# Performance work log

Hardware: AMD Instinct MI355X
Metric: run time of the kernel (lower is better)

The kernel has to match this reference:

```python
import jax, jax.numpy as jnp
import numpy as np

N_EMBD = 1024
N_HEAD = 16
HEAD_SIZE = N_EMBD // N_HEAD  # 64
EPS = 1e-5


def layer_norm(x, gamma, beta):
    mu = jnp.mean(x, axis=-1, keepdims=True)
    var = jnp.var(x, axis=-1, keepdims=True)
    return (x - mu) * jax.lax.rsqrt(var + EPS) * gamma + beta


def setup_inputs() -> dict:
    key = jax.random.key(0)
    ks = jax.random.split(key, 12)
    B, T, C, H, hs = 4, 2048, N_EMBD, N_HEAD, HEAD_SIZE
    s = 0.02
    return {
        "x": jax.random.normal(ks[0], (B, T, C), jnp.float32),
        # per-head projections, stacked over heads: [H, C, hs]
        "Wq": jax.random.normal(ks[1], (H, C, hs), jnp.float32) * s,
        "Wk": jax.random.normal(ks[2], (H, C, hs), jnp.float32) * s,
        "Wv": jax.random.normal(ks[3], (H, C, hs), jnp.float32) * s,
        "Wo": jax.random.normal(ks[4], (C, C), jnp.float32) * s,
        "bo": jnp.zeros((C,), jnp.float32),
        "W1": jax.random.normal(ks[5], (C, 4 * C), jnp.float32) * s,
        "b1": jnp.zeros((4 * C,), jnp.float32),
        "W2": jax.random.normal(ks[6], (4 * C, C), jnp.float32) * s,
        "b2": jnp.zeros((C,), jnp.float32),
        "g1": jnp.ones((C,), jnp.float32),
        "be1": jnp.zeros((C,), jnp.float32),
        "g2": jnp.ones((C,), jnp.float32),
        "be2": jnp.zeros((C,), jnp.float32),
    }


def reference(x, Wq, Wk, Wv, Wo, bo, W1, b1, W2, b2, g1, be1, g2, be2):
    B, T, C = x.shape
    # --- self-attention branch (pre-LN) ---
    h = layer_norm(x, g1, be1)
    q = jnp.einsum("btc,hcd->bhtd", h, Wq)
    k = jnp.einsum("btc,hcd->bhtd", h, Wk)
    v = jnp.einsum("btc,hcd->bhtd", h, Wv)
    scale = HEAD_SIZE ** -0.5
    wei = jnp.einsum("bhtd,bhsd->bhts", q, k) * scale  # [B,H,T,T]
    causal = jnp.tril(jnp.ones((T, T), bool))
    wei = jnp.where(causal, wei, -jnp.inf)
    wei = jax.nn.softmax(wei, axis=-1)
    attn = jnp.einsum("bhts,bhsd->bhtd", wei, v)  # [B,H,T,hs]
    # concat heads -> [B,T,C]
    attn = attn.transpose(0, 2, 1, 3).reshape(B, T, C)
    x = x + attn @ Wo + bo
    # --- MLP branch (pre-LN) ---
    h = layer_norm(x, g2, be2)
    h = jax.nn.relu(h @ W1 + b1) @ W2 + b2
    return x + h
```

## Files before the change

kernel.cpp:

```cpp
#include <hip/hip_runtime.h>
#include <cstdint>
#include <cstddef>


typedef unsigned short u16;
typedef __attribute__((ext_vector_type(8))) __bf16 bf16x8;
typedef __attribute__((ext_vector_type(4))) short s16x4;
typedef __attribute__((ext_vector_type(4))) float f32x4;

#if defined(__has_builtin)
#if __has_builtin(__builtin_amdgcn_global_load_lds)
#define HAS_GLL 1
#endif
#endif

#define QSCALE 0.18033688011112042f

__device__ __forceinline__ u16 f2bf(float f) {
  union { float f; unsigned int u; } c; c.f = f;
  unsigned int u = c.u;
  u += 0x7FFFu + ((u >> 16) & 1u);
  return (u16)(u >> 16);
}
__device__ __forceinline__ u16 f2bf_fast(float f) {
  union { float f; unsigned int u; } c; c.f = f;
  return (u16)((c.u + 0x8000u) >> 16);
}

__device__ __forceinline__ float fexp2(float x) {
#if defined(__HIP_DEVICE_COMPILE__)
#if defined(__has_builtin) && __has_builtin(__builtin_amdgcn_exp2f)
  return __builtin_amdgcn_exp2f(x);
#else
  float r;
  asm("v_exp_f32 %0, %1" : "=v"(r) : "v"(x));
  return r;
#endif
#else
  return x;
#endif
}

__device__ __forceinline__ f32x4 mfma_pv(s16x4 a, s16x4 b, f32x4 c) {
#if defined(__HIP_DEVICE_COMPILE__)
#if defined(__has_builtin) && __has_builtin(__builtin_amdgcn_mfma_f32_16x16x16bf16_1k)
  return __builtin_amdgcn_mfma_f32_16x16x16bf16_1k(a, b, c, 0, 0, 0);
#else
  f32x4 d;
  asm volatile("v_mfma_f32_16x16x16_bf16 %0, %1, %2, %3"
               : "=v"(d) : "v"(a), "v"(b), "v"(c));
  return d;
#endif
#else
  (void)a; (void)b;
  return c;
#endif
}

__device__ __forceinline__ void stage16(const u16* g, u16* l, int lane) {
#ifdef HAS_GLL
  __builtin_amdgcn_global_load_lds(
      (const __attribute__((address_space(1))) uint32_t*)(g),
      (__attribute__((address_space(3))) uint32_t*)(l), 16, 0, 0);
#else
  *(int4*)(l + lane * 8) = *(const int4*)g;
#endif
}

__global__ __launch_bounds__(256) void ln_k(const float* __restrict__ x,
                                            const float* __restrict__ g,
                                            const float* __restrict__ be,
                                            u16* __restrict__ out) {
  const int row = blockIdx.x;
  const int t = threadIdx.x;
  const float4 v = ((const float4*)(x + (size_t)row * 1024))[t];
  float s = v.x + v.y + v.z + v.w;
  float s2 = v.x * v.x + v.y * v.y + v.z * v.z + v.w * v.w;
#pragma unroll
  for (int off = 32; off > 0; off >>= 1) {
    s += __shfl_down(s, off);
    s2 += __shfl_down(s2, off);
  }
  __shared__ float red[8];
  if ((t & 63) == 0) { red[t >> 6] = s; red[4 + (t >> 6)] = s2; }
  __syncthreads();
  const float ts = red[0] + red[1] + red[2] + red[3];
  const float ts2 = red[4] + red[5] + red[6] + red[7];
  const float mu = ts * (1.0f / 1024.0f);
  const float var = ts2 * (1.0f / 1024.0f) - mu * mu;
  const float rstd = rsqrtf(var + 1e-5f);
  const float4 gv = ((const float4*)g)[t];
  const float4 bv = ((const float4*)be)[t];
  u16* op = out + (size_t)row * 1024 + t * 4;
  op[0] = f2bf((v.x - mu) * rstd * gv.x + bv.x);
  op[1] = f2bf((v.y - mu) * rstd * gv.y + bv.y);
  op[2] = f2bf((v.z - mu) * rstd * gv.z + bv.z);
  op[3] = f2bf((v.w - mu) * rstd * gv.w + bv.w);
}

__global__ __launch_bounds__(256) void transpose_k(const float* __restrict__ in,
                                                   u16* __restrict__ out,
                                                   int R, int Cc) {
  __shared__ float tile[32][33];
  const size_t base = (size_t)blockIdx.z * R * Cc;
  const int r0 = blockIdx.x * 32, c0 = blockIdx.y * 32;
  const int tx = threadIdx.x & 31, ty = threadIdx.x >> 5;
  const float* ip = in + base;
  u16* op = out + base;
#pragma unroll
  for (int i = 0; i < 32; i += 8)
    tile[ty + i][tx] = ip[(size_t)(r0 + ty + i) * Cc + c0 + tx];
  __syncthreads();
#pragma unroll
  for (int i = 0; i < 32; i += 8)
    op[(size_t)(c0 + ty + i) * R + r0 + tx] = f2bf(tile[tx][ty + i]);
}

template <int MODE>
__global__ __launch_bounds__(256, 3) void gemm_k(
    const u16* __restrict__ A, const u16* __restrict__ Bt,
    const float* __restrict__ bias, const float* __restrict__ resid,
    void* __restrict__ out0, void* __restrict__ out1, void* __restrict__ out2,
    int M, int N, int K) {
  __shared__ u16 As[128 * 32];
  __shared__ u16 Bs[128 * 32];
  const int tid = threadIdx.x;
  const int lane = tid & 63;
  const int w = tid >> 6;
  const int wm = w & 1, wn = w >> 1;
  const int l15 = lane & 15, lq = lane >> 4;
  const int m0 = blockIdx.x * 128, n0 = blockIdx.y * 128;
  const int srow = lane >> 2, scol = (lane & 3) * 8;

  f32x4 acc[4][4] = {};

  const u16* gA0 = A  + (size_t)(m0 + w * 32 + srow) * K + scol;
  const u16* gA1 = gA0 + (size_t)16 * K;
  const u16* gB0 = Bt + (size_t)(n0 + w * 32 + srow) * K + scol;
  const u16* gB1 = gB0 + (size_t)16 * K;
  u16* lA0 = &As[(w * 32) * 32];
  u16* lA1 = &As[(w * 32 + 16) * 32];
  u16* lB0 = &Bs[(w * 32) * 32];
  u16* lB1 = &Bs[(w * 32 + 16) * 32];

  for (int k0 = 0; k0 < K; k0 += 32) {
    __syncthreads();
    stage16(gA0 + k0, lA0, lane);
    stage16(gA1 + k0, lA1, lane);
    stage16(gB0 + k0, lB0, lane);
    stage16(gB1 + k0, lB1, lane);
    __syncthreads();
    bf16x8 af[4], bfr[4];
#pragma unroll
    for (int i = 0; i < 4; ++i)
      af[i] = *(const bf16x8*)&As[(wm * 64 + i * 16 + l15) * 32 + lq * 8];
#pragma unroll
    for (int j = 0; j < 4; ++j)
      bfr[j] = *(const bf16x8*)&Bs[(wn * 64 + j * 16 + l15) * 32 + lq * 8];
#pragma unroll
    for (int i = 0; i < 4; ++i)
#pragma unroll
      for (int j = 0; j < 4; ++j)
        acc[i][j] = __builtin_amdgcn_mfma_f32_16x16x32_bf16(af[i], bfr[j], acc[i][j], 0, 0, 0);
  }

#pragma unroll
  for (int i = 0; i < 4; ++i) {
    const int mbase = m0 + wm * 64 + i * 16 + lq * 4;
#pragma unroll
    for (int j = 0; j < 4; ++j) {
      const int ncol = n0 + wn * 64 + j * 16 + l15;
#pragma unroll
      for (int r = 0; r < 4; ++r) {
        const float v = acc[i][j][r];
        const int m = mbase + r;
        if (MODE == 0) {
          const int which = ncol >> 10;
          const int hh = (ncol >> 6) & 15;
          const int dd = ncol & 63;
          const int tt = m & 2047;
          const size_t bhb = (size_t)((m >> 11) * 16 + hh) * 131072;
          if (which == 0) {
            ((u16*)out0)[bhb + tt * 64 + dd] = f2bf(v * QSCALE);
          } else if (which == 1) {
            ((u16*)out1)[bhb + (tt >> 4) * 1024 + (dd >> 5) * 512 +
                         ((((dd & 31) >> 3) * 16 + (tt & 15)) << 3) + (dd & 7)] = f2bf(v);
          } else {
            ((u16*)out2)[bhb + (dd >> 4) * 32768 + (tt >> 4) * 256 +
                         (((dd & 15) + (((tt >> 2) & 3)) * 16) << 2) + (tt & 3)] = f2bf(v);
          }
        } else if (MODE == 1 || MODE == 3) {
          ((float*)out0)[(size_t)m * N + ncol] =
              v + bias[ncol] + resid[(size_t)m * N + ncol];
        } else {
          const float t2 = v + bias[ncol];
          ((u16*)out0)[(size_t)m * N + ncol] = f2bf(t2 > 0.0f ? t2 : 0.0f);
        }
      }
    }
  }
}

__global__ __launch_bounds__(256) void flash_k(const u16* __restrict__ q,
                                               const u16* __restrict__ k,
                                               const u16* __restrict__ vt,
                                               u16* __restrict__ attn) {
  const int bh = blockIdx.x;
  const int qblk = 31 - blockIdx.y;
  const int bb = bh >> 4, hh = bh & 15;
  const int tid = threadIdx.x;
  const int lane = tid & 63, wid = tid >> 6;
  const int l15 = lane & 15, lq = lane >> 4;
  const int q0w = qblk * 64 + wid * 16;

  const u16* qrow = q + ((size_t)bh * 2048 + q0w + l15) * 64 + lq * 8;
  const bf16x8 qb0 = *(const bf16x8*)qrow;
  const bf16x8 qb1 = *(const bf16x8*)(qrow + 32);

  const u16* kC = k + (size_t)bh * 131072 + lane * 8;
  const u16* vC = vt + (size_t)bh * 131072 + lane * 4;

  f32x4 o[4] = {};
  float l_acc = 0.0f;

#pragma unroll 4
  for (int j0 = 0; j0 < q0w; j0 += 16) {
    const u16* kp = kC + j0 * 64;
    f32x4 st = {};
    st = __builtin_amdgcn_mfma_f32_16x16x32_bf16(*(const bf16x8*)kp, qb0, st, 0, 0, 0);
    st = __builtin_amdgcn_mfma_f32_16x16x32_bf16(*(const bf16x8*)(kp + 512), qb1, st, 0, 0, 0);

    float p0 = fexp2(st[0]), p1 = fexp2(st[1]);
    float p2 = fexp2(st[2]), p3 = fexp2(st[3]);
    l_acc += (p0 + p1) + (p2 + p3);
    s16x4 pf;
    pf[0] = (short)f2bf_fast(p0); pf[1] = (short)f2bf_fast(p1);
    pf[2] = (short)f2bf_fast(p2); pf[3] = (short)f2bf_fast(p3);

#pragma unroll
    for (int dt = 0; dt < 4; ++dt) {
      const s16x4 va = *(const s16x4*)(vC + dt * 32768 + j0 * 16);
      o[dt] = mfma_pv(va, pf, o[dt]);
    }
  }

  {
    const int j0 = q0w;
    const u16* kp = kC + j0 * 64;
    f32x4 st = {};
    st = __builtin_amdgcn_mfma_f32_16x16x32_bf16(*(const bf16x8*)kp, qb0, st, 0, 0, 0);
    st = __builtin_amdgcn_mfma_f32_16x16x32_bf16(*(const bf16x8*)(kp + 512), qb1, st, 0, 0, 0);
#pragma unroll
    for (int r = 0; r < 4; ++r)
      if (lq * 4 + r > l15) st[r] = -1e30f;

    float p0 = fexp2(st[0]), p1 = fexp2(st[1]);
    float p2 = fexp2(st[2]), p3 = fexp2(st[3]);
    l_acc += (p0 + p1) + (p2 + p3);
    s16x4 pf;
    pf[0] = (short)f2bf_fast(p0); pf[1] = (short)f2bf_fast(p1);
    pf[2] = (short)f2bf_fast(p2); pf[3] = (short)f2bf_fast(p3);

#pragma unroll
    for (int dt = 0; dt < 4; ++dt) {
      const s16x4 va = *(const s16x4*)(vC + dt * 32768 + j0 * 16);
      o[dt] = mfma_pv(va, pf, o[dt]);
    }
  }

  l_acc += __shfl_xor(l_acc, 16);
  l_acc += __shfl_xor(l_acc, 32);
  const float rl = 1.0f / l_acc;

  u16* op = attn + ((size_t)bb * 2048 + q0w + l15) * 1024 + hh * 64 + lq * 4;
#pragma unroll
  for (int dt = 0; dt < 4; ++dt) {
    union { s16x4 v; u16 a[4]; } pk;
#pragma unroll
    for (int r = 0; r < 4; ++r) pk.a[r] = f2bf(o[dt][r] * rl);
    *(s16x4*)(op + dt * 16) = pk.v;
  }
}

extern "C" void kernel_launch(void* const* d_in, const int* in_sizes, int n_in,
                              void* d_out, int out_size, void* d_ws, size_t ws_size,
                              hipStream_t stream) {
  const float* x   = (const float*)d_in[0];
  const float* Wq  = (const float*)d_in[1];
  const float* Wk  = (const float*)d_in[2];
  const float* Wv  = (const float*)d_in[3];
  const float* Wo  = (const float*)d_in[4];
  const float* bo  = (const float*)d_in[5];
  const float* W1  = (const float*)d_in[6];
  const float* b1  = (const float*)d_in[7];
  const float* W2  = (const float*)d_in[8];
  const float* b2  = (const float*)d_in[9];
  const float* g1  = (const float*)d_in[10];
  const float* be1 = (const float*)d_in[11];
  const float* g2  = (const float*)d_in[12];
  const float* be2 = (const float*)d_in[13];
  float* out = (float*)d_out;

  char* ws = (char*)d_ws;
  u16* Wqkv_t = (u16*)(ws + 0);
  u16* Wo_t   = (u16*)(ws + 6291456);
  u16* W1_t   = (u16*)(ws + 8388608);
  u16* W2_t   = (u16*)(ws + 16777216);
  u16* hbuf   = (u16*)(ws + 25165824);
  float* x2   = (float*)(ws + 41943040);
  u16* vtb    = (u16*)(ws + 41943040);
  u16* qb     = (u16*)(ws + 75497472);
  u16* kb     = (u16*)(ws + 92274688);
  u16* attnb  = (u16*)(ws + 109051904);
  u16* a1     = (u16*)(ws + 75497472);

  dim3 blk(256);

  transpose_k<<<dim3(32, 2, 16),  blk, 0, stream>>>(Wq, Wqkv_t,            1024, 64);
  transpose_k<<<dim3(32, 2, 16),  blk, 0, stream>>>(Wk, Wqkv_t + 1048576,  1024, 64);
  transpose_k<<<dim3(32, 2, 16),  blk, 0, stream>>>(Wv, Wqkv_t + 2097152,  1024, 64);
  transpose_k<<<dim3(32, 32, 1),  blk, 0, stream>>>(Wo, Wo_t,              1024, 1024);
  transpose_k<<<dim3(32, 128, 1), blk, 0, stream>>>(W1, W1_t,              1024, 4096);
  transpose_k<<<dim3(128, 32, 1), blk, 0, stream>>>(W2, W2_t,              4096, 1024);

  ln_k<<<8192, blk, 0, stream>>>(x, g1, be1, hbuf);
  gemm_k<0><<<dim3(64, 24), blk, 0, stream>>>(hbuf, Wqkv_t, nullptr, nullptr,
                                              qb, kb, vtb, 8192, 3072, 1024);
  flash_k<<<dim3(64, 32), blk, 0, stream>>>(qb, kb, vtb, attnb);
  gemm_k<1><<<dim3(64, 8), blk, 0, stream>>>(attnb, Wo_t, bo, x,
                                             x2, nullptr, nullptr, 8192, 1024, 1024);
  ln_k<<<8192, blk, 0, stream>>>(x2, g2, be2, hbuf);
  gemm_k<2><<<dim3(64, 32), blk, 0, stream>>>(hbuf, W1_t, b1, nullptr,
                                              a1, nullptr, nullptr, 8192, 4096, 1024);
  gemm_k<3><<<dim3(64, 8), blk, 0, stream>>>(a1, W2_t, b2, x2,
                                             out, nullptr, nullptr, 8192, 1024, 4096);
}
```

Baseline: 530.4 us.

## Process two query tiles per wave in flash attention to reuse K/V loads

Each wave of the flash kernel now handles 32 query rows (two 16-row tiles) instead of 16, so every K and V fragment loaded from global memory feeds two sets of MFMAs. The grid halves along the query dimension and a second diagonal tile is handled separately for the upper query tile. MFMA sections are wrapped in s_setprio hints and launch bounds request 4 blocks per CU. This doubles accumulator register use and produces fewer, larger blocks, which may worsen load balance across the causal triangle.

New measurement: 492.2 us. -7.2%, faster.

```diff
diff --git a/kernel.cpp b/kernel.cpp
--- a/kernel.cpp
+++ b/kernel.cpp
@@ -201,84 +201,162 @@
   }
 }
 
-__global__ __launch_bounds__(256) void flash_k(const u16* __restrict__ q,
-                                               const u16* __restrict__ k,
-                                               const u16* __restrict__ vt,
-                                               u16* __restrict__ attn) {
+__global__ __launch_bounds__(256, 4) void flash_k(const u16* __restrict__ q,
+                                                  const u16* __restrict__ k,
+                                                  const u16* __restrict__ vt,
+                                                  u16* __restrict__ attn) {
   const int bh = blockIdx.x;
-  const int qblk = 31 - blockIdx.y;
+  const int qblk = 15 - blockIdx.y;
   const int bb = bh >> 4, hh = bh & 15;
   const int tid = threadIdx.x;
   const int lane = tid & 63, wid = tid >> 6;
   const int l15 = lane & 15, lq = lane >> 4;
-  const int q0w = qblk * 64 + wid * 16;
-
-  const u16* qrow = q + ((size_t)bh * 2048 + q0w + l15) * 64 + lq * 8;
-  const bf16x8 qb0 = *(const bf16x8*)qrow;
-  const bf16x8 qb1 = *(const bf16x8*)(qrow + 32);
+  const int q0w = qblk * 128 + wid * 32;
+
+  const u16* qrowA = q + ((size_t)bh * 2048 + q0w + l15) * 64 + lq * 8;
+  const bf16x8 qA0 = *(const bf16x8*)qrowA;
+  const bf16x8 qA1 = *(const bf16x8*)(qrowA + 32);
+  const u16* qrowB = qrowA + 16 * 64;
+  const bf16x8 qB0 = *(const bf16x8*)qrowB;
+  const bf16x8 qB1 = *(const bf16x8*)(qrowB + 32);
 
   const u16* kC = k + (size_t)bh * 131072 + lane * 8;
   const u16* vC = vt + (size_t)bh * 131072 + lane * 4;
 
-  f32x4 o[4] = {};
-  float l_acc = 0.0f;
-
-#pragma unroll 4
-  for (int j0 = 0; j0 < q0w; j0 += 16) {
-    const u16* kp = kC + j0 * 64;
-    f32x4 st = {};
-    st = __builtin_amdgcn_mfma_f32_16x16x32_bf16(*(const bf16x8*)kp, qb0, st, 0, 0, 0);
-    st = __builtin_amdgcn_mfma_f32_16x16x32_bf16(*(const bf16x8*)(kp + 512), qb1, st, 0, 0, 0);
-
-    float p0 = fexp2(st[0]), p1 = fexp2(st[1]);
-    float p2 = fexp2(st[2]), p3 = fexp2(st[3]);
-    l_acc += (p0 + p1) + (p2 + p3);
-    s16x4 pf;
-    pf[0] = (short)f2bf_fast(p0); pf[1] = (short)f2bf_fast(p1);
-    pf[2] = (short)f2bf_fast(p2); pf[3] = (short)f2bf_fast(p3);
-
-#pragma unroll
-    for (int dt = 0; dt < 4; ++dt) {
-      const s16x4 va = *(const s16x4*)(vC + dt * 32768 + j0 * 16);
-      o[dt] = mfma_pv(va, pf, o[dt]);
-    }
+  f32x4 oA[4] = {}, oB[4] = {};
+  float lA = 0.0f, lB = 0.0f;
+
+  const int nt = q0w >> 4;
+
+#pragma unroll 2
+  for (int t = 0; t < nt; ++t) {
+    const int ko = t * 1024, vo = t * 256;
+    const bf16x8 ck0 = *(const bf16x8*)(kC + ko);
+    const bf16x8 ck1 = *(const bf16x8*)(kC + ko + 512);
+    const s16x4 cv0 = *(const s16x4*)(vC + vo);
+    const s16x4 cv1 = *(const s16x4*)(vC + vo + 32768);
+    const s16x4 cv2 = *(const s16x4*)(vC + vo + 65536);
+    const s16x4 cv3 = *(const s16x4*)(vC + vo + 98304);
+
+    f32x4 stA = {}, stB = {};
+    __builtin_amdgcn_s_setprio(1);
+    stA = __builtin_amdgcn_mfma_f32_16x16x32_bf16(ck0, qA0, stA, 0, 0, 0);
+    stA = __builtin_amdgcn_mfma_f32_16x16x32_bf16(ck1, qA1, stA, 0, 0, 0);
+    stB = __builtin_amdgcn_mfma_f32_16x16x32_bf16(ck0, qB0, stB, 0, 0, 0);
+    stB = __builtin_amdgcn_mfma_f32_16x16x32_bf16(ck1, qB1, stB, 0, 0, 0);
+    __builtin_amdgcn_s_setprio(0);
+
+    const float a0 = fexp2(stA[0]), a1 = fexp2(stA[1]);
+    const float a2 = fexp2(stA[2]), a3 = fexp2(stA[3]);
+    const float b0 = fexp2(stB[0]), b1 = fexp2(stB[1]);
+    const float b2 = fexp2(stB[2]), b3 = fexp2(stB[3]);
+    lA += (a0 + a1) + (a2 + a3);
+    lB += (b0 + b1) + (b2 + b3);
+    s16x4 pfA, pfB;
+    pfA[0] = (short)f2bf_fast(a0); pfA[1] = (short)f2bf_fast(a1);
+    pfA[2] = (short)f2bf_fast(a2); pfA[3] = (short)f2bf_fast(a3);
+    pfB[0] = (short)f2bf_fast(b0); pfB[1] = (short)f2bf_fast(b1);
+    pfB[2] = (short)f2bf_fast(b2); pfB[3] = (short)f2bf_fast(b3);
+
+    __builtin_amdgcn_s_setprio(1);
+    oA[0] = mfma_pv(cv0, pfA, oA[0]);
+    oA[1] = mfma_pv(cv1, pfA, oA[1]);
+    oA[2] = mfma_pv(cv2, pfA, oA[2]);
+    oA[3] = mfma_pv(cv3, pfA, oA[3]);
+    oB[0] = mfma_pv(cv0, pfB, oB[0]);
+    oB[1] = mfma_pv(cv1, pfB, oB[1]);
+    oB[2] = mfma_pv(cv2, pfB, oB[2]);
+    oB[3] = mfma_pv(cv3, pfB, oB[3]);
+    __builtin_amdgcn_s_setprio(0);
   }
 
   {
-    const int j0 = q0w;
-    const u16* kp = kC + j0 * 64;
-    f32x4 st = {};
-    st = __builtin_amdgcn_mfma_f32_16x16x32_bf16(*(const bf16x8*)kp, qb0, st, 0, 0, 0);
-    st = __builtin_amdgcn_mfma_f32_16x16x32_bf16(*(const bf16x8*)(kp + 512), qb1, st, 0, 0, 0);
+    const int ko = nt * 1024, vo = nt * 256;
+    const bf16x8 ck0 = *(const bf16x8*)(kC + ko);
+    const bf16x8 ck1 = *(const bf16x8*)(kC + ko + 512);
+    const s16x4 cv0 = *(const s16x4*)(vC + vo);
+    const s16x4 cv1 = *(const s16x4*)(vC + vo + 32768);
+    const s16x4 cv2 = *(const s16x4*)(vC + vo + 65536);
+    const s16x4 cv3 = *(const s16x4*)(vC + vo + 98304);
+
+    f32x4 stA = {}, stB = {};
+    stA = __builtin_amdgcn_mfma_f32_16x16x32_bf16(ck0, qA0, stA, 0, 0, 0);
+    stA = __builtin_amdgcn_mfma_f32_16x16x32_bf16(ck1, qA1, stA, 0, 0, 0);
+    stB = __builtin_amdgcn_mfma_f32_16x16x32_bf16(ck0, qB0, stB, 0, 0, 0);
+    stB = __builtin_amdgcn_mfma_f32_16x16x32_bf16(ck1, qB1, stB, 0, 0, 0);
 #pragma unroll
     for (int r = 0; r < 4; ++r)
-      if (lq * 4 + r > l15) st[r] = -1e30f;
-
-    float p0 = fexp2(st[0]), p1 = fexp2(st[1]);
-    float p2 = fexp2(st[2]), p3 = fexp2(st[3]);
-    l_acc += (p0 + p1) + (p2 + p3);
-    s16x4 pf;
-    pf[0] = (short)f2bf_fast(p0); pf[1] = (short)f2bf_fast(p1);
-    pf[2] = (short)f2bf_fast(p2); pf[3] = (short)f2bf_fast(p3);
-
-#pragma unroll
-    for (int dt = 0; dt < 4; ++dt) {
-      const s16x4 va = *(const s16x4*)(vC + dt * 32768 + j0 * 16);
-      o[dt] = mfma_pv(va, pf, o[dt]);
-    }
-  }
-
-  l_acc += __shfl_xor(l_acc, 16);
-  l_acc += __shfl_xor(l_acc, 32);
-  const float rl = 1.0f / l_acc;
-
-  u16* op = attn + ((size_t)bb * 2048 + q0w + l15) * 1024 + hh * 64 + lq * 4;
+      if (lq * 4 + r > l15) stA[r] = -1e30f;
+
+    const float a0 = fexp2(stA[0]), a1 = fexp2(stA[1]);
+    const float a2 = fexp2(stA[2]), a3 = fexp2(stA[3]);
+    const float b0 = fexp2(stB[0]), b1 = fexp2(stB[1]);
+    const float b2 = fexp2(stB[2]), b3 = fexp2(stB[3]);
+    lA += (a0 + a1) + (a2 + a3);
+    lB += (b0 + b1) + (b2 + b3);
+    s16x4 pfA, pfB;
+    pfA[0] = (short)f2bf_fast(a0); pfA[1] = (short)f2bf_fast(a1);
+    pfA[2] = (short)f2bf_fast(a2); pfA[3] = (short)f2bf_fast(a3);
+    pfB[0] = (short)f2bf_fast(b0); pfB[1] = (short)f2bf_fast(b1);
+    pfB[2] = (short)f2bf_fast(b2); pfB[3] = (short)f2bf_fast(b3);
+
+    oA[0] = mfma_pv(cv0, pfA, oA[0]);
+    oA[1] = mfma_pv(cv1, pfA, oA[1]);
+    oA[2] = mfma_pv(cv2, pfA, oA[2]);
+    oA[3] = mfma_pv(cv3, pfA, oA[3]);
+    oB[0] = mfma_pv(cv0, pfB, oB[0]);
+    oB[1] = mfma_pv(cv1, pfB, oB[1]);
+    oB[2] = mfma_pv(cv2, pfB, oB[2]);
+    oB[3] = mfma_pv(cv3, pfB, oB[3]);
+  }
+
+  {
+    const int ko = (nt + 1) * 1024, vo = (nt + 1) * 256;
+    const bf16x8 ck0 = *(const bf16x8*)(kC + ko);
+    const bf16x8 ck1 = *(const bf16x8*)(kC + ko + 512);
+    const s16x4 cv0 = *(const s16x4*)(vC + vo);
+    const s16x4 cv1 = *(const s16x4*)(vC + vo + 32768);
+    const s16x4 cv2 = *(const s16x4*)(vC + vo + 65536);
+    const s16x4 cv3 = *(const s16x4*)(vC + vo + 98304);
+
+    f32x4 stB = {};
+    stB = __builtin_amdgcn_mfma_f32_16x16x32_bf16(ck0, qB0, stB, 0, 0, 0);
+    stB = __builtin_amdgcn_mfma_f32_16x16x32_bf16(ck1, qB1, stB, 0, 0, 0);
+#pragma unroll
+    for (int r = 0; r < 4; ++r)
+      if (lq * 4 + r > l15) stB[r] = -1e30f;
+
+    const float b0 = fexp2(stB[0]), b1 = fexp2(stB[1]);
+    const float b2 = fexp2(stB[2]), b3 = fexp2(stB[3]);
+    lB += (b0 + b1) + (b2 + b3);
+    s16x4 pfB;
+    pfB[0] = (short)f2bf_fast(b0); pfB[1] = (short)f2bf_fast(b1);
+    pfB[2] = (short)f2bf_fast(b2); pfB[3] = (short)f2bf_fast(b3);
+
+    oB[0] = mfma_pv(cv0, pfB, oB[0]);
+    oB[1] = mfma_pv(cv1, pfB, oB[1]);
+    oB[2] = mfma_pv(cv2, pfB, oB[2]);
+    oB[3] = mfma_pv(cv3, pfB, oB[3]);
+  }
+
+  lA += __shfl_xor(lA, 16);
+  lA += __shfl_xor(lA, 32);
+  lB += __shfl_xor(lB, 16);
+  lB += __shfl_xor(lB, 32);
+  const float rlA = 1.0f / lA;
+  const float rlB = 1.0f / lB;
+
+  u16* opA = attn + ((size_t)bb * 2048 + q0w + l15) * 1024 + hh * 64 + lq * 4;
+  u16* opB = opA + 16 * 1024;
 #pragma unroll
   for (int dt = 0; dt < 4; ++dt) {
     union { s16x4 v; u16 a[4]; } pk;
 #pragma unroll
-    for (int r = 0; r < 4; ++r) pk.a[r] = f2bf(o[dt][r] * rl);
-    *(s16x4*)(op + dt * 16) = pk.v;
+    for (int r = 0; r < 4; ++r) pk.a[r] = f2bf(oA[dt][r] * rlA);
+    *(s16x4*)(opA + dt * 16) = pk.v;
+#pragma unroll
+    for (int r = 0; r < 4; ++r) pk.a[r] = f2bf(oB[dt][r] * rlB);
+    *(s16x4*)(opB + dt * 16) = pk.v;
   }
 }
 
@@ -326,7 +404,7 @@
   ln_k<<<8192, blk, 0, stream>>>(x, g1, be1, hbuf);
   gemm_k<0><<<dim3(64, 24), blk, 0, stream>>>(hbuf, Wqkv_t, nullptr, nullptr,
                                               qb, kb, vtb, 8192, 3072, 1024);
-  flash_k<<<dim3(64, 32), blk, 0, stream>>>(qb, kb, vtb, attnb);
+  flash_k<<<dim3(64, 16), blk, 0, stream>>>(qb, kb, vtb, attnb);
   gemm_k<1><<<dim3(64, 8), blk, 0, stream>>>(attnb, Wo_t, bo, x,
                                              x2, nullptr, nullptr, 8192, 1024, 1024);
   ln_k<<<8192, blk, 0, stream>>>(x2, g2, be2, hbuf);
```
